# Optimization experiments

Hardware: AMD Instinct MI355X
Metric: run time of the kernel (lower is better)

Reference implementation:

```python
import jax, jax.numpy as jnp
import numpy as np

N = 500000
D = 112
H = 64
W = 176


def setup_inputs() -> dict:
    key = jax.random.key(0)
    k1, k2 = jax.random.split(key)
    # positions: x in [0, W-1), y in [0, H-1)
    u = jax.random.uniform(k1, (N, 2), dtype=jnp.float32)
    sampling_positions = u * jnp.array([W - 1.0, H - 1.0], dtype=jnp.float32)
    sampling_depth_features = jax.random.normal(k2, (N, D), dtype=jnp.float32)
    return {
        "sampling_positions": sampling_positions,
        "sampling_depth_features": sampling_depth_features,
        "height": H,
        "width": W,
    }


def _bilinear_scatter(positions, features, height, width):
    # positions: [N,2] (x, y); features: [N,D] -> grid [H,W,D]
    x = positions[:, 0]
    y = positions[:, 1]
    x0 = jnp.floor(x)
    y0 = jnp.floor(y)
    wx = x - x0
    wy = y - y0
    x0i = x0.astype(jnp.int32)
    y0i = y0.astype(jnp.int32)
    x1i = x0i + 1
    y1i = y0i + 1

    out = jnp.zeros((height, width, features.shape[1]), dtype=jnp.float32)

    def in_bounds(yi, xi):
        return (yi >= 0) & (yi < height) & (xi >= 0) & (xi < width)

    corners = [
        (y0i, x0i, (1.0 - wy) * (1.0 - wx)),
        (y0i, x1i, (1.0 - wy) * wx),
        (y1i, x0i, wy * (1.0 - wx)),
        (y1i, x1i, wy * wx),
    ]
    for yi, xi, w in corners:
        valid = in_bounds(yi, xi)
        w = jnp.where(valid, w, 0.0)
        yi = jnp.clip(yi, 0, height - 1)
        xi = jnp.clip(xi, 0, width - 1)
        out = out.at[yi, xi].add(w[:, None] * features)
    return out


def reference(sampling_positions, sampling_depth_features, height, width):
    return _bilinear_scatter(sampling_positions, sampling_depth_features, height, width)
```

## Files before the change

### kernel.cpp

```cpp
#include <hip/hip_runtime.h>


#define D     112
#define D2    56
#define H     64
#define W     176
#define HW    (H * W)
#define CAP   128
#define CSTR  16
#define TY    4
#define TX    4
#define GX    (W / TX)
#define GY    (H / TY)
#define NCELL (TY * TX)
#define NW    8
#define NBIN  25
#define NSLOT (NBIN * CAP)

__device__ __forceinline__ void fill_one(int p, float x, float y,
                                         int* cnt, uint2* bucket)
{
    float xf = floorf(x), yf = floorf(y);
    float wx = x - xf,    wy = y - yf;
    int x0 = min(max((int)xf, 0), W - 1);
    int y0 = min(max((int)yf, 0), H - 1);
    int bin = y0 * W + x0;
    unsigned qw = (__float2uint_rn(wy * 65535.0f) << 16)
                |  __float2uint_rn(wx * 65535.0f);
    int i = atomicAdd(&cnt[bin * CSTR], 1);
    if (i < CAP) bucket[(size_t)bin * CAP + i] = make_uint2((unsigned)p, qw);
}

__global__ __launch_bounds__(256) void fill_kernel(
    const float2* __restrict__ pos,
    int* __restrict__ cnt,
    uint2* __restrict__ bucket,
    int N)
{
    int i = blockIdx.x * blockDim.x + threadIdx.x;
    int p0 = 4 * i;
    if (p0 >= N) return;
    const float4* p4 = (const float4*)pos;
    if (p0 + 3 < N) {
        float4 a = p4[2 * i];
        float4 b = p4[2 * i + 1];
        fill_one(p0,     a.x, a.y, cnt, bucket);
        fill_one(p0 + 1, a.z, a.w, cnt, bucket);
        fill_one(p0 + 2, b.x, b.y, cnt, bucket);
        fill_one(p0 + 3, b.z, b.w, cnt, bucket);
    } else {
        for (int k = 0; k < 4 && p0 + k < N; ++k) {
            float2 q = pos[p0 + k];
            fill_one(p0 + k, q.x, q.y, cnt, bucket);
        }
    }
}

__global__ __launch_bounds__(512, 6) void accum_kernel(
    const float* __restrict__ feat,
    const int* __restrict__ cnt,
    const uint2* __restrict__ bucket,
    float* __restrict__ out)
{
    const int tile = blockIdx.x;
    const int ty0  = (tile / GX) * TY;
    const int tx0  = (tile % GX) * TX;
    const int t    = threadIdx.x;
    const int wid  = t >> 6;
    const int lane = t & 63;
    const bool act = lane < D2;

    __shared__ int sn[NBIN];
    __shared__ __align__(16) char smem[NSLOT * sizeof(uint2)];
    uint2* shdr = (uint2*)smem;

    if (t < NBIN) {
        int by = t / 5 - 1, bx = t % 5 - 1;
        int gby = ty0 + by, gbx = tx0 + bx;
        int n = 0;
        if (gby >= 0 && gbx >= 0 && gbx < W)
            n = min(cnt[(gby * W + gbx) * CSTR], CAP);
        sn[t] = n;
    }
    __syncthreads();

    for (int i = t; i < NSLOT; i += 512) {
        int b = i >> 7, s = i & (CAP - 1);
        if (s < sn[b]) {
            int by = b / 5 - 1, bx = b % 5 - 1;
            int gbin = (ty0 + by) * W + (tx0 + bx);
            shdr[i] = bucket[(size_t)gbin * CAP + s];
        }
    }
    __syncthreads();

    float2 acc[NCELL];
#pragma unroll
    for (int c = 0; c < NCELL; ++c) acc[c] = make_float2(0.0f, 0.0f);

#pragma unroll
    for (int by = -1; by < TY; ++by) {
#pragma unroll
        for (int bx = -1; bx < TX; ++bx) {
            const int b  = (by + 1) * 5 + (bx + 1);
            const int n  = sn[b];
            const int lo = (n * wid) >> 3;
            const int hi = (n * (wid + 1)) >> 3;
            const uint2* hb = shdr + b * CAP;

#pragma unroll 4
            for (int e = lo; e < hi; ++e) {
                uint2 en = hb[e];
                float wx = (float)(en.y & 0xffffu) * (1.0f / 65535.0f);
                float wy = (float)(en.y >> 16)     * (1.0f / 65535.0f);
                float2 f = make_float2(0.0f, 0.0f);
                if (act)
                    f = ((const float2*)(feat + (size_t)en.x * D))[lane];
                float ax = 1.0f - wx, ay = 1.0f - wy;
#pragma unroll
                for (int dy = 0; dy < 2; ++dy) {
                    const int cy = by + dy;
                    if (cy < 0 || cy >= TY) continue;
                    const float fy = dy ? wy : ay;
#pragma unroll
                    for (int dx = 0; dx < 2; ++dx) {
                        const int cx = bx + dx;
                        if (cx < 0 || cx >= TX) continue;
                        const float fw = fy * (dx ? wx : ax);
                        const int c = cy * TX + cx;
                        acc[c].x = fmaf(fw, f.x, acc[c].x);
                        acc[c].y = fmaf(fw, f.y, acc[c].y);
                    }
                }
            }
        }
    }

    __syncthreads();
    float2 (*sacc)[NCELL][D2] = reinterpret_cast<float2 (*)[NCELL][D2]>(smem);
    const int half = wid >> 2;
    const int sub  = wid & 3;

    for (int w = 0; w < 4; ++w) {
        if (sub == w && act) {
            if (w == 0) {
#pragma unroll
                for (int c = 0; c < NCELL; ++c) sacc[half][c][lane] = acc[c];
            } else {
#pragma unroll
                for (int c = 0; c < NCELL; ++c) {
                    float2 v = sacc[half][c][lane];
                    v.x += acc[c].x; v.y += acc[c].y;
                    sacc[half][c][lane] = v;
                }
            }
        }
        __syncthreads();
    }

    if (act) {
#pragma unroll
        for (int k = 0; k < 2; ++k) {
            const int c  = wid * 2 + k;
            const int cy = c / TX, cx = c % TX;
            float2 v0 = sacc[0][c][lane];
            float2 v1 = sacc[1][c][lane];
            float2* dst = (float2*)(out + ((size_t)(ty0 + cy) * W + (tx0 + cx)) * D);
            dst[lane] = make_float2(v0.x + v1.x, v0.y + v1.y);
        }
    }
}

extern "C" void kernel_launch(void* const* d_in, const int* in_sizes, int n_in,
                              void* d_out, int out_size, void* d_ws, size_t ws_size,
                              hipStream_t stream) {
    const float2* pos = (const float2*)d_in[0];
    const float* feat = (const float*)d_in[1];
    float* out        = (float*)d_out;

    const int N = in_sizes[0] / 2;

    int* cnt      = (int*)d_ws;
    uint2* bucket = (uint2*)((char*)d_ws + (size_t)HW * CSTR * sizeof(int));

    hipMemsetAsync(cnt, 0, (size_t)HW * CSTR * sizeof(int), stream);

    int nq = (N + 3) / 4;
    fill_kernel<<<(nq + 255) / 256, 256, 0, stream>>>(pos, cnt, bucket, N);

    accum_kernel<<<GY * GX, 512, 0, stream>>>(feat, cnt, bucket, out);
}
```

Measured before the change: 364.2 us.

## Double accum block to 16 waves and batch four feature-row loads per iteration

The accumulation kernel now runs 1024 threads (16 waves) per tile, so each bin's entries are split 16 ways instead of 8. The inner loop is restructured to issue up to four header reads and four feature-row global loads before doing the FMAs, so more memory requests are in flight at once. The shared-memory reduction now uses four partial copies in a union with the header buffer, and the final pass sums them. The tradeoffs are more registers per thread under the new launch bounds, extra reduction rounds, and fewer entries per wave when bins are sparse.

```diff
diff --git a/kernel.cpp b/kernel.cpp
--- a/kernel.cpp
+++ b/kernel.cpp
@@ -13,7 +13,7 @@
 #define GX    (W / TX)
 #define GY    (H / TY)
 #define NCELL (TY * TX)
-#define NW    8
+#define NW    16
 #define NBIN  25
 #define NSLOT (NBIN * CAP)
 
@@ -56,7 +56,7 @@
     }
 }
 
-__global__ __launch_bounds__(512, 6) void accum_kernel(
+__global__ __launch_bounds__(1024, 8) void accum_kernel(
     const float* __restrict__ feat,
     const int* __restrict__ cnt,
     const uint2* __restrict__ bucket,
@@ -71,8 +71,10 @@
     const bool act = lane < D2;
 
     __shared__ int sn[NBIN];
-    __shared__ __align__(16) char smem[NSLOT * sizeof(uint2)];
-    uint2* shdr = (uint2*)smem;
+    __shared__ __align__(16) union {
+        uint2  hdr[NSLOT];
+        float2 sacc[4][NCELL][D2];
+    } sm;
 
     if (t < NBIN) {
         int by = t / 5 - 1, bx = t % 5 - 1;
@@ -84,12 +86,12 @@
     }
     __syncthreads();
 
-    for (int i = t; i < NSLOT; i += 512) {
+    for (int i = t; i < NSLOT; i += 1024) {
         int b = i >> 7, s = i & (CAP - 1);
         if (s < sn[b]) {
             int by = b / 5 - 1, bx = b % 5 - 1;
             int gbin = (ty0 + by) * W + (tx0 + bx);
-            shdr[i] = bucket[(size_t)gbin * CAP + s];
+            sm.hdr[i] = bucket[(size_t)gbin * CAP + s];
         }
     }
     __syncthreads();
@@ -104,18 +106,13 @@
         for (int bx = -1; bx < TX; ++bx) {
             const int b  = (by + 1) * 5 + (bx + 1);
             const int n  = sn[b];
-            const int lo = (n * wid) >> 3;
-            const int hi = (n * (wid + 1)) >> 3;
-            const uint2* hb = shdr + b * CAP;
-
-#pragma unroll 4
-            for (int e = lo; e < hi; ++e) {
-                uint2 en = hb[e];
+            const int lo = (n * wid) >> 4;
+            const int hi = (n * (wid + 1)) >> 4;
+            const uint2* hb = sm.hdr + b * CAP;
+
+            auto proc = [&](uint2 en, float2 f) {
                 float wx = (float)(en.y & 0xffffu) * (1.0f / 65535.0f);
                 float wy = (float)(en.y >> 16)     * (1.0f / 65535.0f);
-                float2 f = make_float2(0.0f, 0.0f);
-                if (act)
-                    f = ((const float2*)(feat + (size_t)en.x * D))[lane];
                 float ax = 1.0f - wx, ay = 1.0f - wy;
 #pragma unroll
                 for (int dy = 0; dy < 2; ++dy) {
@@ -132,42 +129,63 @@
                         acc[c].y = fmaf(fw, f.y, acc[c].y);
                     }
                 }
+            };
+            auto ldrow = [&](unsigned p) -> float2 {
+                return act ? ((const float2*)(feat + (size_t)p * D))[lane]
+                           : make_float2(0.0f, 0.0f);
+            };
+
+            for (int e0 = lo; e0 < hi; e0 += 4) {
+                const int m = hi - e0;
+                uint2 h0, h1, h2, h3;
+                float2 f0, f1, f2, f3;
+                h0 = hb[e0];
+                if (m > 1) h1 = hb[e0 + 1];
+                if (m > 2) h2 = hb[e0 + 2];
+                if (m > 3) h3 = hb[e0 + 3];
+                f0 = ldrow(h0.x);
+                if (m > 1) f1 = ldrow(h1.x);
+                if (m > 2) f2 = ldrow(h2.x);
+                if (m > 3) f3 = ldrow(h3.x);
+                proc(h0, f0);
+                if (m > 1) proc(h1, f1);
+                if (m > 2) proc(h2, f2);
+                if (m > 3) proc(h3, f3);
             }
         }
     }
 
     __syncthreads();
-    float2 (*sacc)[NCELL][D2] = reinterpret_cast<float2 (*)[NCELL][D2]>(smem);
-    const int half = wid >> 2;
-    const int sub  = wid & 3;
+    const int copy = wid & 3;
+    const int rnd  = wid >> 2;
 
     for (int w = 0; w < 4; ++w) {
-        if (sub == w && act) {
+        if (rnd == w && act) {
             if (w == 0) {
 #pragma unroll
-                for (int c = 0; c < NCELL; ++c) sacc[half][c][lane] = acc[c];
+                for (int c = 0; c < NCELL; ++c) sm.sacc[copy][c][lane] = acc[c];
             } else {
 #pragma unroll
                 for (int c = 0; c < NCELL; ++c) {
-                    float2 v = sacc[half][c][lane];
+                    float2 v = sm.sacc[copy][c][lane];
                     v.x += acc[c].x; v.y += acc[c].y;
-                    sacc[half][c][lane] = v;
+                    sm.sacc[copy][c][lane] = v;
                 }
             }
         }
         __syncthreads();
     }
 
-    if (act) {
-#pragma unroll
-        for (int k = 0; k < 2; ++k) {
-            const int c  = wid * 2 + k;
-            const int cy = c / TX, cx = c % TX;
-            float2 v0 = sacc[0][c][lane];
-            float2 v1 = sacc[1][c][lane];
-            float2* dst = (float2*)(out + ((size_t)(ty0 + cy) * W + (tx0 + cx)) * D);
-            dst[lane] = make_float2(v0.x + v1.x, v0.y + v1.y);
-        }
+    if (wid < NCELL && act) {
+        const int c  = wid;
+        const int cy = c / TX, cx = c % TX;
+        float2 v0 = sm.sacc[0][c][lane];
+        float2 v1 = sm.sacc[1][c][lane];
+        float2 v2 = sm.sacc[2][c][lane];
+        float2 v3 = sm.sacc[3][c][lane];
+        float2* dst = (float2*)(out + ((size_t)(ty0 + cy) * W + (tx0 + cx)) * D);
+        dst[lane] = make_float2((v0.x + v1.x) + (v2.x + v3.x),
+                                (v0.y + v1.y) + (v2.y + v3.y));
     }
 }
 
@@ -188,5 +206,5 @@
     int nq = (N + 3) / 4;
     fill_kernel<<<(nq + 255) / 256, 256, 0, stream>>>(pos, cnt, bucket, N);
 
-    accum_kernel<<<GY * GX, 512, 0, stream>>>(feat, cnt, bucket, out);
-}
+    accum_kernel<<<GY * GX, 1024, 0, stream>>>(feat, cnt, bucket, out);
+}
```

After: 366.7 us. No clear change (+0.7%).

## Shrink accumulation tile to 2x2 cells with 256-thread blocks

Applied to the files above, without the earlier changes.

Changes the gather/accumulate kernel from 4x4-cell tiles with 512 threads to 2x2-cell tiles with 256 threads, each thread owning one feature channel and four cell accumulators. Two half-blocks split bucket entries and combine through a single shared-memory exchange. This cuts register and shared-memory use per block, raises block count and simplifies the reduction. The cost is more halo overlap, so each feature row is re-read from global memory more often, and loads are scalar instead of float2.

```diff
diff --git a/kernel.cpp b/kernel.cpp
--- a/kernel.cpp
+++ b/kernel.cpp
@@ -2,20 +2,14 @@
 
 
 #define D     112
-#define D2    56
 #define H     64
 #define W     176
 #define HW    (H * W)
 #define CAP   128
 #define CSTR  16
-#define TY    4
-#define TX    4
-#define GX    (W / TX)
-#define GY    (H / TY)
-#define NCELL (TY * TX)
-#define NW    8
-#define NBIN  25
-#define NSLOT (NBIN * CAP)
+#define GX2   (W / 2)
+#define GY2   (H / 2)
+#define NBIN9 9
 
 __device__ __forceinline__ void fill_one(int p, float x, float y,
                                          int* cnt, uint2* bucket)
@@ -56,80 +50,70 @@
     }
 }
 
-__global__ __launch_bounds__(512, 6) void accum_kernel(
+__global__ __launch_bounds__(256, 8) void accum_kernel(
     const float* __restrict__ feat,
     const int* __restrict__ cnt,
     const uint2* __restrict__ bucket,
     float* __restrict__ out)
 {
     const int tile = blockIdx.x;
-    const int ty0  = (tile / GX) * TY;
-    const int tx0  = (tile % GX) * TX;
+    const int ty0  = (tile / GX2) * 2;
+    const int tx0  = (tile % GX2) * 2;
     const int t    = threadIdx.x;
-    const int wid  = t >> 6;
-    const int lane = t & 63;
-    const bool act = lane < D2;
+    const int h    = t >> 7;
+    const int c    = t & 127;
+    const bool act = c < D;
 
-    __shared__ int sn[NBIN];
-    __shared__ __align__(16) char smem[NSLOT * sizeof(uint2)];
-    uint2* shdr = (uint2*)smem;
+    __shared__ int   sn[NBIN9];
+    __shared__ uint2 se[NBIN9][CAP];
+    __shared__ float sacc[4][D];
 
-    if (t < NBIN) {
-        int by = t / 5 - 1, bx = t % 5 - 1;
+    if (t < NBIN9) {
+        int by = t / 3 - 1, bx = t % 3 - 1;
         int gby = ty0 + by, gbx = tx0 + bx;
         int n = 0;
-        if (gby >= 0 && gbx >= 0 && gbx < W)
+        if (gby >= 0 && gby < H && gbx >= 0 && gbx < W)
             n = min(cnt[(gby * W + gbx) * CSTR], CAP);
         sn[t] = n;
     }
     __syncthreads();
 
-    for (int i = t; i < NSLOT; i += 512) {
-        int b = i >> 7, s = i & (CAP - 1);
-        if (s < sn[b]) {
-            int by = b / 5 - 1, bx = b % 5 - 1;
+    for (int i = t; i < NBIN9 * CAP; i += 256) {
+        int b = i >> 7, e = i & (CAP - 1);
+        if (e < sn[b]) {
+            int by = b / 3 - 1, bx = b % 3 - 1;
             int gbin = (ty0 + by) * W + (tx0 + bx);
-            shdr[i] = bucket[(size_t)gbin * CAP + s];
+            se[b][e] = bucket[(size_t)gbin * CAP + e];
         }
     }
     __syncthreads();
 
-    float2 acc[NCELL];
-#pragma unroll
-    for (int c = 0; c < NCELL; ++c) acc[c] = make_float2(0.0f, 0.0f);
+    float acc[4] = {0.0f, 0.0f, 0.0f, 0.0f};
 
 #pragma unroll
-    for (int by = -1; by < TY; ++by) {
+    for (int by = -1; by <= 1; ++by) {
 #pragma unroll
-        for (int bx = -1; bx < TX; ++bx) {
-            const int b  = (by + 1) * 5 + (bx + 1);
-            const int n  = sn[b];
-            const int lo = (n * wid) >> 3;
-            const int hi = (n * (wid + 1)) >> 3;
-            const uint2* hb = shdr + b * CAP;
-
-#pragma unroll 4
-            for (int e = lo; e < hi; ++e) {
-                uint2 en = hb[e];
+        for (int bx = -1; bx <= 1; ++bx) {
+            const int b = (by + 1) * 3 + (bx + 1);
+            const int n = sn[b];
+#pragma unroll 8
+            for (int e = h; e < n; e += 2) {
+                uint2 en = se[b][e];
                 float wx = (float)(en.y & 0xffffu) * (1.0f / 65535.0f);
                 float wy = (float)(en.y >> 16)     * (1.0f / 65535.0f);
-                float2 f = make_float2(0.0f, 0.0f);
-                if (act)
-                    f = ((const float2*)(feat + (size_t)en.x * D))[lane];
+                float f  = act ? feat[(size_t)en.x * D + c] : 0.0f;
                 float ax = 1.0f - wx, ay = 1.0f - wy;
 #pragma unroll
                 for (int dy = 0; dy < 2; ++dy) {
                     const int cy = by + dy;
-                    if (cy < 0 || cy >= TY) continue;
+                    if (cy < 0 || cy > 1) continue;
                     const float fy = dy ? wy : ay;
 #pragma unroll
                     for (int dx = 0; dx < 2; ++dx) {
                         const int cx = bx + dx;
-                        if (cx < 0 || cx >= TX) continue;
-                        const float fw = fy * (dx ? wx : ax);
-                        const int c = cy * TX + cx;
-                        acc[c].x = fmaf(fw, f.x, acc[c].x);
-                        acc[c].y = fmaf(fw, f.y, acc[c].y);
+                        if (cx < 0 || cx > 1) continue;
+                        acc[cy * 2 + cx] =
+                            fmaf(fy * (dx ? wx : ax), f, acc[cy * 2 + cx]);
                     }
                 }
             }
@@ -137,36 +121,17 @@
     }
 
     __syncthreads();
-    float2 (*sacc)[NCELL][D2] = reinterpret_cast<float2 (*)[NCELL][D2]>(smem);
-    const int half = wid >> 2;
-    const int sub  = wid & 3;
-
-    for (int w = 0; w < 4; ++w) {
-        if (sub == w && act) {
-            if (w == 0) {
+    if (h == 1 && act) {
 #pragma unroll
-                for (int c = 0; c < NCELL; ++c) sacc[half][c][lane] = acc[c];
-            } else {
+        for (int cell = 0; cell < 4; ++cell) sacc[cell][c] = acc[cell];
+    }
+    __syncthreads();
+    if (h == 0 && act) {
 #pragma unroll
-                for (int c = 0; c < NCELL; ++c) {
-                    float2 v = sacc[half][c][lane];
-                    v.x += acc[c].x; v.y += acc[c].y;
-                    sacc[half][c][lane] = v;
-                }
-            }
-        }
-        __syncthreads();
-    }
-
-    if (act) {
-#pragma unroll
-        for (int k = 0; k < 2; ++k) {
-            const int c  = wid * 2 + k;
-            const int cy = c / TX, cx = c % TX;
-            float2 v0 = sacc[0][c][lane];
-            float2 v1 = sacc[1][c][lane];
-            float2* dst = (float2*)(out + ((size_t)(ty0 + cy) * W + (tx0 + cx)) * D);
-            dst[lane] = make_float2(v0.x + v1.x, v0.y + v1.y);
+        for (int cell = 0; cell < 4; ++cell) {
+            const int cy = cell >> 1, cx = cell & 1;
+            out[((size_t)(ty0 + cy) * W + (tx0 + cx)) * D + c]
+                = acc[cell] + sacc[cell][c];
         }
     }
 }
@@ -188,5 +153,5 @@
     int nq = (N + 3) / 4;
     fill_kernel<<<(nq + 255) / 256, 256, 0, stream>>>(pos, cnt, bucket, N);
 
-    accum_kernel<<<GY * GX, 512, 0, stream>>>(feat, cnt, bucket, out);
+    accum_kernel<<<GY2 * GX2, 256, 0, stream>>>(feat, cnt, bucket, out);
 }
```

After: 391.0 us. +7.4%, slower.
